# Kernel tuning notes

Measured on AMD Instinct MI355X. Metric: run time of the kernel, lower is better.

The kernel has to match this reference:

```python
import jax, jax.numpy as jnp
import numpy as np

N_T, N_Q = 32768, 4096
E_T, E_Q = 1048576, 131072
H = 128
VOCAB = 1001  # num_features + 1
NUM_LAYERS = 3


def _sage_conv(x, edge_index, Wl, bl, Wr):
    # PyG SAGEConv, aggr='mean': out = lin_l(mean_j x_j) + lin_r(x_i)
    src, dst = edge_index[0], edge_index[1]
    n = x.shape[0]
    agg = jax.ops.segment_sum(x[src], dst, num_segments=n)          # [n, H]
    cnt = jax.ops.segment_sum(jnp.ones((src.shape[0],), x.dtype), dst, num_segments=n)
    mean = agg / jnp.maximum(cnt, 1.0)[:, None]
    return mean @ Wl.T + bl + x @ Wr.T


def setup_inputs() -> dict:
    key = jax.random.key(0)
    ks = jax.random.split(key, 12)
    target_x = jax.random.randint(ks[0], (N_T,), 0, VOCAB, dtype=jnp.int64 if jax.config.jax_enable_x64 else jnp.int32)
    query_x = jax.random.randint(ks[1], (N_Q,), 0, VOCAB, dtype=target_x.dtype)
    target_edge_index = jax.random.randint(ks[2], (2, E_T), 0, N_T, dtype=target_x.dtype)
    query_edge_index = jax.random.randint(ks[3], (2, E_Q), 0, N_Q, dtype=target_x.dtype)
    mask = jax.random.bernoulli(ks[4], 0.5, (N_Q, N_T))
    emb = jax.random.normal(ks[5], (VOCAB, H), jnp.float32) * 0.02
    s = 1.0 / np.sqrt(H)
    Wl = jax.random.uniform(ks[6], (NUM_LAYERS, H, H), jnp.float32, -s, s)
    bl = jax.random.uniform(ks[7], (NUM_LAYERS, H), jnp.float32, -s, s)
    Wr = jax.random.uniform(ks[8], (NUM_LAYERS, H, H), jnp.float32, -s, s)
    return {"target_x": target_x, "query_x": query_x,
            "target_edge_index": target_edge_index, "query_edge_index": query_edge_index,
            "mask": mask, "emb": emb, "Wl": Wl, "bl": bl, "Wr": Wr}


def reference(target_x, query_x, target_edge_index, query_edge_index, mask, emb, Wl, bl, Wr):
    et = emb[target_x]  # [N_T, H]
    eq = emb[query_x]   # [N_Q, H]
    for i in range(NUM_LAYERS):
        et = jax.nn.elu(_sage_conv(et, target_edge_index, Wl[i], bl[i], Wr[i]))
        eq = jax.nn.elu(_sage_conv(eq, query_edge_index, Wl[i], bl[i], Wr[i]))
    fmask = mask.astype(jnp.float32)
    att = (eq @ et.T) * fmask / jnp.sqrt(jnp.float32(H)) + (-1e9) * (1.0 - fmask)
    att = jax.nn.softmax(att, axis=1)
    return att[None]  # [1, N_Q, N_T]
```

## Files before the change

kernel.cpp:

```cpp
#include <hip/hip_runtime.h>
#include <stdint.h>

#define N_T 32768
#define N_Q 4096
#define E_T 1048576
#define E_Q 131072
#define H   128
#define NL  3

typedef float    f32x4 __attribute__((ext_vector_type(4)));
typedef _Float16 f16x8 __attribute__((ext_vector_type(8)));

__device__ __forceinline__ ushort f2h(float x){
  union{_Float16 h; ushort u;} c; c.h = (_Float16)x; return c.u;
}
__device__ __forceinline__ float h2f(unsigned u){
  union{ushort u; _Float16 h;} c; c.u = (ushort)u; return (float)c.h;
}

__global__ void zero_i32_k(int* p, int n){
  int i = blockIdx.x*blockDim.x + threadIdx.x;
  if(i<n) p[i]=0;
}
__global__ void zero_f32_k(float* p, int n){
  int i = blockIdx.x*blockDim.x + threadIdx.x;
  if(i<n) p[i]=0.f;
}

__global__ void detect_mask_k(const unsigned* m, int* flag){
  int t = threadIdx.x;
  int f = 0;
  for(int j=t;j<4096;j+=256){
    unsigned v = m[j];
    if(v > 1u) f |= (v & 0xFEFEFEFEu) ? 2 : 1;
  }
  if(f) atomicOr(flag, f);
}

__global__ void wcvt_k(const float* __restrict__ Wl, const float* __restrict__ Wr,
                       ushort* __restrict__ WH, ushort* __restrict__ WLo){
  int i = blockIdx.x*blockDim.x + threadIdx.x;
  if(i >= NL*128*64) return;
  int k  = (i & 63) * 4;
  int c  = (i >> 6) & 127;
  int l  = i >> 13;
  const float* src = (k < 128)
      ? &Wl[((size_t)l*128 + c)*128 + k]
      : &Wr[((size_t)l*128 + c)*128 + (k-128)];
  float4 v = *(const float4*)src;
  ushort4 h, lo;
  h.x = f2h(v.x); lo.x = f2h(v.x - h2f(h.x));
  h.y = f2h(v.y); lo.y = f2h(v.y - h2f(h.y));
  h.z = f2h(v.z); lo.z = f2h(v.z - h2f(h.z));
  h.w = f2h(v.w); lo.w = f2h(v.w - h2f(h.w));
  size_t off = ((size_t)l*128 + c)*256 + k;
  *(ushort4*)&WH[off]  = h;
  *(ushort4*)&WLo[off] = lo;
}

__global__ void count_k(const int* __restrict__ dst, int E, int* cnt){
  int i = blockIdx.x*blockDim.x + threadIdx.x;
  if(i<E) atomicAdd(&cnt[dst[i]], 1);
}

__global__ void scan_k(const int* __restrict__ cnt, int n, int* rp, int* pos){
  __shared__ int part[1024];
  int t = threadIdx.x;
  int chunk = (n + 1023) >> 10;
  int lo = t*chunk, hi = lo+chunk; if(hi>n) hi=n;
  int s = 0;
  for(int i=lo;i<hi;i++) s += cnt[i];
  part[t] = s;
  __syncthreads();
  for(int off=1; off<1024; off<<=1){
    int v = (t >= off) ? part[t-off] : 0;
    __syncthreads();
    part[t] += v;
    __syncthreads();
  }
  int run = (t==0) ? 0 : part[t-1];
  for(int i=lo;i<hi;i++){ rp[i]=run; pos[i]=run; run += cnt[i]; }
  if(t==0) rp[n] = part[1023];
}

__global__ void fill_k(const int* __restrict__ src, const int* __restrict__ dst,
                       int E, int* pos, int* csr){
  int i = blockIdx.x*blockDim.x + threadIdx.x;
  if(i<E){
    int p = atomicAdd(&pos[dst[i]], 1);
    csr[p] = src[i];
  }
}

__global__ void embed_k(const int* __restrict__ idx, const float* __restrict__ emb,
                        ushort* __restrict__ out, int N){
  int i = blockIdx.x*blockDim.x + threadIdx.x;
  int n = i >> 4, c = i & 15;
  if(n < N){
    size_t eb = (size_t)idx[n]*32 + c*2;
    float4 v0 = ((const float4*)emb)[eb];
    float4 v1 = ((const float4*)emb)[eb+1];
    uint4 o;
    o.x = (unsigned)f2h(v0.x) | ((unsigned)f2h(v0.y)<<16);
    o.y = (unsigned)f2h(v0.z) | ((unsigned)f2h(v0.w)<<16);
    o.z = (unsigned)f2h(v1.x) | ((unsigned)f2h(v1.y)<<16);
    o.w = (unsigned)f2h(v1.z) | ((unsigned)f2h(v1.w)<<16);
    ((uint4*)out)[(size_t)n*16 + c] = o;
  }
}

__global__ void agg_k(const ushort* __restrict__ x, const int* __restrict__ rp,
                      const int* __restrict__ csr, ushort* __restrict__ agg, int N){
  int wid = (int)(((size_t)blockIdx.x*blockDim.x + threadIdx.x) >> 6);
  int lane = threadIdx.x & 63;
  if(wid >= N) return;
  const unsigned* xp = (const unsigned*)x;
  int rs = rp[wid], re = rp[wid+1];
  float ax=0.f, ay=0.f, bx=0.f, by=0.f, cx=0.f, cy=0.f, dx=0.f, dy=0.f;
  int j = rs;
  for(; j+4 <= re; j+=4){
    int s0 = csr[j], s1 = csr[j+1], s2 = csr[j+2], s3 = csr[j+3];
    unsigned u0 = xp[(size_t)s0*64 + lane];
    unsigned u1 = xp[(size_t)s1*64 + lane];
    unsigned u2 = xp[(size_t)s2*64 + lane];
    unsigned u3 = xp[(size_t)s3*64 + lane];
    ax += h2f(u0 & 0xFFFFu); ay += h2f(u0 >> 16);
    bx += h2f(u1 & 0xFFFFu); by += h2f(u1 >> 16);
    cx += h2f(u2 & 0xFFFFu); cy += h2f(u2 >> 16);
    dx += h2f(u3 & 0xFFFFu); dy += h2f(u3 >> 16);
  }
  for(; j < re; j++){
    unsigned u = xp[(size_t)csr[j]*64 + lane];
    ax += h2f(u & 0xFFFFu); ay += h2f(u >> 16);
  }
  float sx = (ax + bx) + (cx + dx);
  float sy = (ay + by) + (cy + dy);
  int c = re - rs; if(c < 1) c = 1;
  float inv = 1.0f / (float)c;
  ((unsigned*)agg)[(size_t)wid*64 + lane] =
      (unsigned)f2h(sx*inv) | ((unsigned)f2h(sy*inv) << 16);
}

__global__ __launch_bounds__(256,3) void layer_k(
    const ushort* __restrict__ agg, const ushort* __restrict__ x,
    const ushort* __restrict__ WH, const ushort* __restrict__ WLo,
    const float* __restrict__ bl, ushort* __restrict__ out16){
  __shared__ ushort SM3[3*128*64];
  ushort* SA = SM3;
  ushort* SH = SM3 + 8192;
  ushort* SL = SM3 + 16384;
  int t = threadIdx.x;
  int r0g = blockIdx.x * 128;
  int lane = t & 63;
  int w = t >> 6;
  int wr = w >> 1, wc = w & 1;
  int fr = lane & 15, kg0 = lane >> 4;
  f32x4 acc[4][4] = {};
  for(int kt=0; kt<4; kt++){
    __syncthreads();
    const ushort* A = (kt < 2) ? agg : x;
    int ko = (kt & 1) * 64;
    #pragma unroll
    for(int it=0; it<4; it++){
      int idx = t + it*256;
      int row = idx >> 3, k8 = idx & 7;
      int sw = (k8 ^ (row & 7)) * 8;
      *(uint4*)&SA[row*64 + sw] = *(const uint4*)&A[(size_t)(r0g+row)*H + ko + k8*8];
      *(uint4*)&SH[row*64 + sw] = *(const uint4*)&WH[row*256 + kt*64 + k8*8];
      *(uint4*)&SL[row*64 + sw] = *(const uint4*)&WLo[row*256 + kt*64 + k8*8];
    }
    __syncthreads();
    #pragma unroll
    for(int s=0; s<2; s++){
      int kg = s*4 + kg0;
      f16x8 a[4], bh[4], blo[4];
      #pragma unroll
      for(int m=0;m<4;m++){
        int ar = wr*64 + m*16 + fr;
        a[m] = *(const f16x8*)&SA[ar*64 + ((kg ^ (ar & 7)) << 3)];
      }
      #pragma unroll
      for(int n=0;n<4;n++){
        int bc = wc*64 + n*16 + fr;
        int ib = bc*64 + ((kg ^ (bc & 7)) << 3);
        bh[n]  = *(const f16x8*)&SH[ib];
        blo[n] = *(const f16x8*)&SL[ib];
      }
      #pragma unroll
      for(int m=0;m<4;m++)
        #pragma unroll
        for(int n=0;n<4;n++){
          acc[m][n] = __builtin_amdgcn_mfma_f32_16x16x32_f16(a[m], bh[n],  acc[m][n], 0,0,0);
          acc[m][n] = __builtin_amdgcn_mfma_f32_16x16x32_f16(a[m], blo[n], acc[m][n], 0,0,0);
        }
    }
  }
  __syncthreads();
  ushort* LT = SM3;
  #pragma unroll
  for(int n=0;n<4;n++){
    int c = wc*64 + n*16 + fr;
    float b = bl[c];
    #pragma unroll
    for(int m=0;m<4;m++){
      int r = wr*64 + m*16 + kg0*4;
      #pragma unroll
      for(int reg=0;reg<4;reg++){
        float v = acc[m][n][reg] + b;
        v = (v > 0.f) ? v : expm1f(v);
        LT[(r+reg)*128 + c] = f2h(v);
      }
    }
  }
  __syncthreads();
  #pragma unroll
  for(int i=0;i<8;i++){
    int idx = t + i*256;
    int row = idx >> 4, c8 = idx & 15;
    *(uint4*)&out16[(size_t)(r0g+row)*H + c8*8] = *(uint4*)&LT[row*128 + c8*8];
  }
}

__device__ __forceinline__ unsigned nib8(unsigned x, unsigned y){
  unsigned r = (x & 0xFu) | ((x>>4)&0xF0u) | ((x>>8)&0xF00u) | ((x>>12)&0xF000u);
  unsigned s = (y & 0xFu) | ((y>>4)&0xF0u) | ((y>>8)&0xF00u) | ((y>>12)&0xF000u);
  return r | (s<<16);
}
__device__ __forceinline__ unsigned pk4(unsigned u){
  return ((u & 0xFFu)       ? 1u : 0u) | ((u & 0xFF00u)     ? 2u : 0u)
       | ((u & 0xFF0000u)   ? 4u : 0u) | ((u & 0xFF000000u) ? 8u : 0u);
}

__device__ __forceinline__ void stage_mask_tile(const void* maskp, int mb,
    int gr0, int gc0, unsigned* MB, uint8_t* NB, unsigned* bitsOut, int t){
  if(mb & 2){
    const float* base = (const float*)maskp;
    #pragma unroll
    for(int i=0;i<16;i++){
      int idx = i*256 + t;
      int row = idx >> 5, c4 = idx & 31;
      float4 v = *(const float4*)&base[(size_t)(gr0+row)*N_T + gc0 + c4*4];
      NB[row*32 + c4] = (uint8_t)((unsigned)(v.x!=0.f) | ((unsigned)(v.y!=0.f)<<1)
                                | ((unsigned)(v.z!=0.f)<<2) | ((unsigned)(v.w!=0.f)<<3));
    }
  } else if(mb & 1){
    const uint8_t* base = (const uint8_t*)maskp;
    #pragma unroll
    for(int i=0;i<16;i++){
      int idx = i*256 + t;
      int row = idx >> 5, c4 = idx & 31;
      unsigned u = *(const unsigned*)&base[(size_t)(gr0+row)*N_T + gc0 + c4*4];
      NB[row*32 + c4] = (uint8_t)pk4(u);
    }
  } else {
    const int* base = (const int*)maskp;
    #pragma unroll
    for(int i=0;i<16;i++){
      int idx = i*256 + t;
      int row = idx >> 5, c4 = idx & 31;
      int4 v = *(const int4*)&base[(size_t)(gr0+row)*N_T + gc0 + c4*4];
      NB[row*32 + c4] = (uint8_t)((unsigned)(v.x!=0) | ((unsigned)(v.y!=0)<<1)
                                | ((unsigned)(v.z!=0)<<2) | ((unsigned)(v.w!=0)<<3));
    }
  }
  __syncthreads();
  if(t < 128){
    uint4 a = *(const uint4*)&NB[t*32];
    uint4 b = *(const uint4*)&NB[t*32 + 16];
    unsigned w0 = nib8(a.x, a.y), w1 = nib8(a.z, a.w);
    unsigned w2 = nib8(b.x, b.y), w3 = nib8(b.z, b.w);
    MB[t*4]   = w0; MB[t*4+1] = w1;
    MB[t*4+2] = w2; MB[t*4+3] = w3;
    if(bitsOut){
      uint4 o; o.x=w0; o.y=w1; o.z=w2; o.w=w3;
      *(uint4*)&bitsOut[(size_t)(gr0 + t)*(N_T/32) + (gc0 >> 5)] = o;
    }
  }
}

__device__ __forceinline__ void qk_gemm(
    const ushort* __restrict__ A16, const ushort* __restrict__ B16,
    int abase, int bbase, int t, ushort* SM, f32x4 (&acc)[4][4]){
  ushort* AB = SM;
  ushort* BB = SM + 8192;
  int lane = t & 63;
  int w = t >> 6;
  int wr = w >> 1, wc = w & 1;
  int fr = lane & 15, kg0 = lane >> 4;
  for(int kt=0; kt<2; kt++){
    __syncthreads();
    #pragma unroll
    for(int it=0; it<4; it++){
      int idx = t + it*256;
      int row = idx >> 3, k8 = idx & 7;
      int sw = (k8 ^ (row & 7)) * 8;
      *(uint4*)&AB[row*64 + sw] = *(const uint4*)&A16[(size_t)(abase+row)*H + kt*64 + k8*8];
      *(uint4*)&BB[row*64 + sw] = *(const uint4*)&B16[(size_t)(bbase+row)*H + kt*64 + k8*8];
    }
    __syncthreads();
    #pragma unroll
    for(int s=0; s<2; s++){
      int kg = s*4 + kg0;
      f16x8 a[4], b[4];
      #pragma unroll
      for(int m=0;m<4;m++){
        int ar = wr*64 + m*16 + fr;
        a[m] = *(const f16x8*)&AB[ar*64 + ((kg ^ (ar & 7)) << 3)];
      }
      #pragma unroll
      for(int n=0;n<4;n++){
        int bc = wc*64 + n*16 + fr;
        b[n] = *(const f16x8*)&BB[bc*64 + ((kg ^ (bc & 7)) << 3)];
      }
      #pragma unroll
      for(int m=0;m<4;m++)
        #pragma unroll
        for(int n=0;n<4;n++)
          acc[m][n] = __builtin_amdgcn_mfma_f32_16x16x32_f16(a[m], b[n], acc[m][n], 0,0,0);
    }
  }
}

__global__ __launch_bounds__(256,4) void attsum_k(
    const ushort* __restrict__ eq16, const ushort* __restrict__ et16,
    const void* __restrict__ maskp, const int* __restrict__ flag,
    unsigned* __restrict__ bitsOut, float* __restrict__ rowsum){
  __shared__ ushort SM[2*128*64];
  __shared__ __align__(16) unsigned MB[512];
  __shared__ float RS[128][2];
  int t = threadIdx.x;
  int gc0 = blockIdx.x * 128;
  int gr0 = blockIdx.y * 128;
  int lane = t & 63;
  int w = t >> 6;
  int wr = w >> 1, wc = w & 1;
  int fr = lane & 15, kg0 = lane >> 4;

  int mb = *flag;
  stage_mask_tile(maskp, mb, gr0, gc0, MB, (uint8_t*)SM, bitsOut, t);

  f32x4 acc[4][4] = {};
  qk_gemm(et16, eq16, gc0, gr0, t, SM, acc);

  const float sc = 0.08838834764831845f;
  #pragma unroll
  for(int n=0;n<4;n++){
    int q = wc*64 + n*16 + fr;
    float s = 0.f;
    #pragma unroll
    for(int m=0;m<4;m++){
      unsigned wb = MB[q*4 + wr*2 + (m>>1)];
      int off = ((m&1)<<4) | (kg0<<2);
      s += ((wb>>(off+0))&1u) ? __expf(acc[m][n][0]*sc) : 0.f;
      s += ((wb>>(off+1))&1u) ? __expf(acc[m][n][1]*sc) : 0.f;
      s += ((wb>>(off+2))&1u) ? __expf(acc[m][n][2]*sc) : 0.f;
      s += ((wb>>(off+3))&1u) ? __expf(acc[m][n][3]*sc) : 0.f;
    }
    s += __shfl_xor(s, 16);
    s += __shfl_xor(s, 32);
    if(lane < 16) RS[q][wr] = s;
  }
  __syncthreads();
  if(t < 128) atomicAdd(&rowsum[gr0 + t], RS[t][0] + RS[t][1]);
}

__global__ __launch_bounds__(256,4) void attout_k(
    const ushort* __restrict__ eq16, const ushort* __restrict__ et16,
    const void* __restrict__ maskp, const int* __restrict__ flag,
    const unsigned* __restrict__ bitsIn, const float* __restrict__ rowsum,
    float* __restrict__ out){
  __shared__ ushort SM[2*128*64];
  __shared__ __align__(16) unsigned MB[512];
  __shared__ float IRS[128];
  int t = threadIdx.x;
  int gc0 = blockIdx.x * 128;
  int gr0 = blockIdx.y * 128;
  int lane = t & 63;
  int w = t >> 6;
  int wr = w >> 1, wc = w & 1;
  int fr = lane & 15, kg0 = lane >> 4;

  if(bitsIn){
    if(t < 128)
      *(uint4*)&MB[t*4] = *(const uint4*)&bitsIn[(size_t)(gr0 + t)*(N_T/32) + (gc0 >> 5)];
  } else {
    int mb = *flag;
    stage_mask_tile(maskp, mb, gr0, gc0, MB, (uint8_t*)SM, nullptr, t);
  }
  if(t < 128) IRS[t] = 1.0f / rowsum[gr0 + t];

  f32x4 acc[4][4] = {};
  qk_gemm(et16, eq16, gc0, gr0, t, SM, acc);

  const float sc = 0.08838834764831845f;
  #pragma unroll
  for(int n=0;n<4;n++){
    int q = wc*64 + n*16 + fr;
    float ir = IRS[q];
    size_t rb = (size_t)(gr0 + q)*N_T + gc0 + wr*64;
    #pragma unroll
    for(int m=0;m<4;m++){
      unsigned wb = MB[q*4 + wr*2 + (m>>1)];
      int off = ((m&1)<<4) | (kg0<<2);
      float4 o;
      o.x = ((wb>>(off+0))&1u) ? __expf(acc[m][n][0]*sc)*ir : 0.f;
      o.y = ((wb>>(off+1))&1u) ? __expf(acc[m][n][1]*sc)*ir : 0.f;
      o.z = ((wb>>(off+2))&1u) ? __expf(acc[m][n][2]*sc)*ir : 0.f;
      o.w = ((wb>>(off+3))&1u) ? __expf(acc[m][n][3]*sc)*ir : 0.f;
      *(float4*)&out[rb + m*16 + (kg0<<2)] = o;
    }
  }
}

extern "C" void kernel_launch(void* const* d_in, const int* in_sizes, int n_in,
                              void* d_out, int out_size, void* d_ws, size_t ws_size,
                              hipStream_t stream){
  const int* tx  = (const int*)d_in[0];
  const int* qx  = (const int*)d_in[1];
  const int* te  = (const int*)d_in[2];
  const int* qe  = (const int*)d_in[3];
  const void* mask = d_in[4];
  const float* emb = (const float*)d_in[5];
  const float* Wl  = (const float*)d_in[6];
  const float* bl  = (const float*)d_in[7];
  const float* Wr  = (const float*)d_in[8];
  float* out = (float*)d_out;

  ushort* et16 = (ushort*)d_ws;
  ushort* eq16 = et16 + (size_t)N_T*H;
  float* rowsum = (float*)(eq16 + (size_t)N_Q*H);
  int*   flag   = (int*)(rowsum + N_Q);
  ushort* WH  = (ushort*)((char*)d_ws + ((size_t)10 << 20));
  ushort* WLo = WH + (size_t)NL*128*256;
  bool useBits = ws_size >= ((size_t)37 << 20);
  unsigned* bits = useBits ? (unsigned*)((char*)d_ws + ((size_t)19 << 20)) : nullptr;

  char* S = (char*)d_out;
  ushort* xt0  = (ushort*)(S);
  ushort* xt1  = (ushort*)(S + 8388608);
  ushort* aggt = (ushort*)(S + 16777216);
  ushort* xq0  = (ushort*)(S + 25165824);
  ushort* xq1  = (ushort*)(S + 26214400);
  ushort* aggq = (ushort*)(S + 27262976);
  int*   cnt_t = (int*)(S + 28311552);
  int*   rp_t  = cnt_t + N_T;
  int*   pos_t = rp_t + N_T + 1;
  int*   csr_t = pos_t + N_T;
  int*   cnt_q = csr_t + E_T;
  int*   rp_q  = cnt_q + N_Q;
  int*   pos_q = rp_q + N_Q + 1;
  int*   csr_q = pos_q + N_Q;

  zero_i32_k<<<(N_T+255)/256,256,0,stream>>>(cnt_t, N_T);
  zero_i32_k<<<(N_Q+255)/256,256,0,stream>>>(cnt_q, N_Q);
  zero_f32_k<<<(N_Q+255)/256,256,0,stream>>>(rowsum, N_Q);
  zero_i32_k<<<1,256,0,stream>>>(flag, 1);
  detect_mask_k<<<1,256,0,stream>>>((const unsigned*)mask, flag);
  wcvt_k<<<96,256,0,stream>>>(Wl, Wr, WH, WLo);

  count_k<<<E_T/256,256,0,stream>>>(te+E_T, E_T, cnt_t);
  scan_k<<<1,1024,0,stream>>>(cnt_t, N_T, rp_t, pos_t);
  fill_k<<<E_T/256,256,0,stream>>>(te, te+E_T, E_T, pos_t, csr_t);
  count_k<<<E_Q/256,256,0,stream>>>(qe+E_Q, E_Q, cnt_q);
  scan_k<<<1,1024,0,stream>>>(cnt_q, N_Q, rp_q, pos_q);
  fill_k<<<E_Q/256,256,0,stream>>>(qe, qe+E_Q, E_Q, pos_q, csr_q);

  embed_k<<<N_T*16/256,256,0,stream>>>(tx, emb, xt0, N_T);
  embed_k<<<N_Q*16/256,256,0,stream>>>(qx, emb, xq0, N_Q);

  ushort* ct = xt0; ushort* nt = xt1;
  ushort* cq = xq0; ushort* nq = xq1;
  for(int l=0;l<NL;l++){
    int last = (l == NL-1);
    const ushort* wh = WH  + (size_t)l*128*256;
    const ushort* wl = WLo + (size_t)l*128*256;
    agg_k<<<N_T/4,256,0,stream>>>(ct, rp_t, csr_t, aggt, N_T);
    layer_k<<<N_T/128,256,0,stream>>>(aggt, ct, wh, wl, bl+(size_t)l*H, last ? et16 : nt);
    agg_k<<<N_Q/4,256,0,stream>>>(cq, rp_q, csr_q, aggq, N_Q);
    layer_k<<<N_Q/128,256,0,stream>>>(aggq, cq, wh, wl, bl+(size_t)l*H, last ? eq16 : nq);
    ushort* tmp;
    tmp = ct; ct = nt; nt = tmp;
    tmp = cq; cq = nq; nq = tmp;
  }

  attsum_k<<<dim3(N_T/128, N_Q/128),256,0,stream>>>(eq16, et16, mask, flag, bits, rowsum);
  attout_k<<<dim3(N_T/128, N_Q/128),256,0,stream>>>(eq16, et16, mask, flag, bits, rowsum, out);
}
```

Measured before the change: 766.8 us.

## Fuse embedding lookup into layer-0 gather, widen agg unroll, use nontemporal mask/output

Drops the per-node embed kernels. Layer 0 instead gathers rows straight from a small fp16 copy of the embedding table, indexed by node id, in both the aggregation and the layer GEMM. The aggregation loop now unrolls over 8 neighbours with separate accumulators, which gives more memory-level parallelism. Mask loads and output stores in the attention kernels become nontemporal, so the large streaming traffic bypasses cache retention. The costs are a double indirection in layer 0 and the rowsum buffer moving to a new workspace offset.

```diff
diff --git a/kernel.cpp b/kernel.cpp
--- a/kernel.cpp
+++ b/kernel.cpp
@@ -7,8 +7,11 @@
 #define E_Q 131072
 #define H   128
 #define NL  3
+#define VOCAB 1001
 
 typedef float    f32x4 __attribute__((ext_vector_type(4)));
+typedef int      i32x4 __attribute__((ext_vector_type(4)));
+typedef unsigned u32x4 __attribute__((ext_vector_type(4)));
 typedef _Float16 f16x8 __attribute__((ext_vector_type(8)));
 
 __device__ __forceinline__ ushort f2h(float x){
@@ -58,6 +61,19 @@
   *(ushort4*)&WLo[off] = lo;
 }
 
+__global__ void ecvt_k(const float* __restrict__ e, ushort* __restrict__ o){
+  int i = blockIdx.x*blockDim.x + threadIdx.x;
+  if(i >= VOCAB*H/8) return;
+  float4 v0 = ((const float4*)e)[(size_t)i*2];
+  float4 v1 = ((const float4*)e)[(size_t)i*2 + 1];
+  uint4 u;
+  u.x = (unsigned)f2h(v0.x) | ((unsigned)f2h(v0.y)<<16);
+  u.y = (unsigned)f2h(v0.z) | ((unsigned)f2h(v0.w)<<16);
+  u.z = (unsigned)f2h(v1.x) | ((unsigned)f2h(v1.y)<<16);
+  u.w = (unsigned)f2h(v1.z) | ((unsigned)f2h(v1.w)<<16);
+  ((uint4*)o)[i] = u;
+}
+
 __global__ void count_k(const int* __restrict__ dst, int E, int* cnt){
   int i = blockIdx.x*blockDim.x + threadIdx.x;
   if(i<E) atomicAdd(&cnt[dst[i]], 1);
@@ -92,49 +108,47 @@
   }
 }
 
-__global__ void embed_k(const int* __restrict__ idx, const float* __restrict__ emb,
-                        ushort* __restrict__ out, int N){
-  int i = blockIdx.x*blockDim.x + threadIdx.x;
-  int n = i >> 4, c = i & 15;
-  if(n < N){
-    size_t eb = (size_t)idx[n]*32 + c*2;
-    float4 v0 = ((const float4*)emb)[eb];
-    float4 v1 = ((const float4*)emb)[eb+1];
-    uint4 o;
-    o.x = (unsigned)f2h(v0.x) | ((unsigned)f2h(v0.y)<<16);
-    o.y = (unsigned)f2h(v0.z) | ((unsigned)f2h(v0.w)<<16);
-    o.z = (unsigned)f2h(v1.x) | ((unsigned)f2h(v1.y)<<16);
-    o.w = (unsigned)f2h(v1.z) | ((unsigned)f2h(v1.w)<<16);
-    ((uint4*)out)[(size_t)n*16 + c] = o;
-  }
-}
-
-__global__ void agg_k(const ushort* __restrict__ x, const int* __restrict__ rp,
-                      const int* __restrict__ csr, ushort* __restrict__ agg, int N){
+__global__ void agg_k(const ushort* __restrict__ x, const int* __restrict__ nid,
+                      const ushort* __restrict__ emb16,
+                      const int* __restrict__ rp, const int* __restrict__ csr,
+                      ushort* __restrict__ agg, int N){
   int wid = (int)(((size_t)blockIdx.x*blockDim.x + threadIdx.x) >> 6);
   int lane = threadIdx.x & 63;
   if(wid >= N) return;
-  const unsigned* xp = (const unsigned*)x;
+  const unsigned* xw = (const unsigned*)x;
+  const unsigned* ew = (const unsigned*)emb16;
   int rs = rp[wid], re = rp[wid+1];
-  float ax=0.f, ay=0.f, bx=0.f, by=0.f, cx=0.f, cy=0.f, dx=0.f, dy=0.f;
+  float px[8], py[8];
+  #pragma unroll
+  for(int q=0;q<8;q++){ px[q]=0.f; py[q]=0.f; }
   int j = rs;
-  for(; j+4 <= re; j+=4){
-    int s0 = csr[j], s1 = csr[j+1], s2 = csr[j+2], s3 = csr[j+3];
-    unsigned u0 = xp[(size_t)s0*64 + lane];
-    unsigned u1 = xp[(size_t)s1*64 + lane];
-    unsigned u2 = xp[(size_t)s2*64 + lane];
-    unsigned u3 = xp[(size_t)s3*64 + lane];
-    ax += h2f(u0 & 0xFFFFu); ay += h2f(u0 >> 16);
-    bx += h2f(u1 & 0xFFFFu); by += h2f(u1 >> 16);
-    cx += h2f(u2 & 0xFFFFu); cy += h2f(u2 >> 16);
-    dx += h2f(u3 & 0xFFFFu); dy += h2f(u3 >> 16);
-  }
-  for(; j < re; j++){
-    unsigned u = xp[(size_t)csr[j]*64 + lane];
-    ax += h2f(u & 0xFFFFu); ay += h2f(u >> 16);
-  }
-  float sx = (ax + bx) + (cx + dx);
-  float sy = (ay + by) + (cy + dy);
+  if(nid){
+    for(; j+8 <= re; j+=8){
+      #pragma unroll
+      for(int q=0;q<8;q++){
+        unsigned u = ew[(size_t)nid[csr[j+q]]*64 + lane];
+        px[q] += h2f(u & 0xFFFFu); py[q] += h2f(u >> 16);
+      }
+    }
+    for(; j < re; j++){
+      unsigned u = ew[(size_t)nid[csr[j]]*64 + lane];
+      px[0] += h2f(u & 0xFFFFu); py[0] += h2f(u >> 16);
+    }
+  } else {
+    for(; j+8 <= re; j+=8){
+      #pragma unroll
+      for(int q=0;q<8;q++){
+        unsigned u = xw[(size_t)csr[j+q]*64 + lane];
+        px[q] += h2f(u & 0xFFFFu); py[q] += h2f(u >> 16);
+      }
+    }
+    for(; j < re; j++){
+      unsigned u = xw[(size_t)csr[j]*64 + lane];
+      px[0] += h2f(u & 0xFFFFu); py[0] += h2f(u >> 16);
+    }
+  }
+  float sx = ((px[0]+px[1]) + (px[2]+px[3])) + ((px[4]+px[5]) + (px[6]+px[7]));
+  float sy = ((py[0]+py[1]) + (py[2]+py[3])) + ((py[4]+py[5]) + (py[6]+py[7]));
   int c = re - rs; if(c < 1) c = 1;
   float inv = 1.0f / (float)c;
   ((unsigned*)agg)[(size_t)wid*64 + lane] =
@@ -142,7 +156,8 @@
 }
 
 __global__ __launch_bounds__(256,3) void layer_k(
-    const ushort* __restrict__ agg, const ushort* __restrict__ x,
+    const ushort* __restrict__ agg, const ushort* __restrict__ xprev,
+    const int* __restrict__ nid, const ushort* __restrict__ emb16,
     const ushort* __restrict__ WH, const ushort* __restrict__ WLo,
     const float* __restrict__ bl, ushort* __restrict__ out16){
   __shared__ ushort SM3[3*128*64];
@@ -158,14 +173,21 @@
   f32x4 acc[4][4] = {};
   for(int kt=0; kt<4; kt++){
     __syncthreads();
-    const ushort* A = (kt < 2) ? agg : x;
     int ko = (kt & 1) * 64;
     #pragma unroll
     for(int it=0; it<4; it++){
       int idx = t + it*256;
       int row = idx >> 3, k8 = idx & 7;
       int sw = (k8 ^ (row & 7)) * 8;
-      *(uint4*)&SA[row*64 + sw] = *(const uint4*)&A[(size_t)(r0g+row)*H + ko + k8*8];
+      uint4 av;
+      if(kt < 2){
+        av = *(const uint4*)&agg[(size_t)(r0g+row)*H + ko + k8*8];
+      } else if(nid){
+        av = *(const uint4*)&emb16[(size_t)nid[r0g+row]*H + ko + k8*8];
+      } else {
+        av = *(const uint4*)&xprev[(size_t)(r0g+row)*H + ko + k8*8];
+      }
+      *(uint4*)&SA[row*64 + sw] = av;
       *(uint4*)&SH[row*64 + sw] = *(const uint4*)&WH[row*256 + kt*64 + k8*8];
       *(uint4*)&SL[row*64 + sw] = *(const uint4*)&WLo[row*256 + kt*64 + k8*8];
     }
@@ -234,14 +256,15 @@
 __device__ __forceinline__ void stage_mask_tile(const void* maskp, int mb,
     int gr0, int gc0, unsigned* MB, uint8_t* NB, unsigned* bitsOut, int t){
   if(mb & 2){
-    const float* base = (const float*)maskp;
+    const f32x4* base = (const f32x4*)maskp;
     #pragma unroll
     for(int i=0;i<16;i++){
       int idx = i*256 + t;
       int row = idx >> 5, c4 = idx & 31;
-      float4 v = *(const float4*)&base[(size_t)(gr0+row)*N_T + gc0 + c4*4];
-      NB[row*32 + c4] = (uint8_t)((unsigned)(v.x!=0.f) | ((unsigned)(v.y!=0.f)<<1)
-                                | ((unsigned)(v.z!=0.f)<<2) | ((unsigned)(v.w!=0.f)<<3));
+      f32x4 v = __builtin_nontemporal_load(
+          &base[((size_t)(gr0+row)*N_T + gc0) / 4 + c4]);
+      NB[row*32 + c4] = (uint8_t)((unsigned)(v[0]!=0.f) | ((unsigned)(v[1]!=0.f)<<1)
+                                | ((unsigned)(v[2]!=0.f)<<2) | ((unsigned)(v[3]!=0.f)<<3));
     }
   } else if(mb & 1){
     const uint8_t* base = (const uint8_t*)maskp;
@@ -249,18 +272,20 @@
     for(int i=0;i<16;i++){
       int idx = i*256 + t;
       int row = idx >> 5, c4 = idx & 31;
-      unsigned u = *(const unsigned*)&base[(size_t)(gr0+row)*N_T + gc0 + c4*4];
+      unsigned u = __builtin_nontemporal_load(
+          (const unsigned*)&base[(size_t)(gr0+row)*N_T + gc0 + c4*4]);
       NB[row*32 + c4] = (uint8_t)pk4(u);
     }
   } else {
-    const int* base = (const int*)maskp;
+    const i32x4* base = (const i32x4*)maskp;
     #pragma unroll
     for(int i=0;i<16;i++){
       int idx = i*256 + t;
       int row = idx >> 5, c4 = idx & 31;
-      int4 v = *(const int4*)&base[(size_t)(gr0+row)*N_T + gc0 + c4*4];
-      NB[row*32 + c4] = (uint8_t)((unsigned)(v.x!=0) | ((unsigned)(v.y!=0)<<1)
-                                | ((unsigned)(v.z!=0)<<2) | ((unsigned)(v.w!=0)<<3));
+      i32x4 v = __builtin_nontemporal_load(
+          &base[((size_t)(gr0+row)*N_T + gc0) / 4 + c4]);
+      NB[row*32 + c4] = (uint8_t)((unsigned)(v[0]!=0) | ((unsigned)(v[1]!=0)<<1)
+                                | ((unsigned)(v[2]!=0)<<2) | ((unsigned)(v[3]!=0)<<3));
     }
   }
   __syncthreads();
@@ -402,12 +427,12 @@
     for(int m=0;m<4;m++){
       unsigned wb = MB[q*4 + wr*2 + (m>>1)];
       int off = ((m&1)<<4) | (kg0<<2);
-      float4 o;
-      o.x = ((wb>>(off+0))&1u) ? __expf(acc[m][n][0]*sc)*ir : 0.f;
-      o.y = ((wb>>(off+1))&1u) ? __expf(acc[m][n][1]*sc)*ir : 0.f;
-      o.z = ((wb>>(off+2))&1u) ? __expf(acc[m][n][2]*sc)*ir : 0.f;
-      o.w = ((wb>>(off+3))&1u) ? __expf(acc[m][n][3]*sc)*ir : 0.f;
-      *(float4*)&out[rb + m*16 + (kg0<<2)] = o;
+      f32x4 o;
+      o[0] = ((wb>>(off+0))&1u) ? __expf(acc[m][n][0]*sc)*ir : 0.f;
+      o[1] = ((wb>>(off+1))&1u) ? __expf(acc[m][n][1]*sc)*ir : 0.f;
+      o[2] = ((wb>>(off+2))&1u) ? __expf(acc[m][n][2]*sc)*ir : 0.f;
+      o[3] = ((wb>>(off+3))&1u) ? __expf(acc[m][n][3]*sc)*ir : 0.f;
+      __builtin_nontemporal_store(o, (f32x4*)&out[rb + m*16 + (kg0<<2)]);
     }
   }
 }
@@ -428,10 +453,11 @@
 
   ushort* et16 = (ushort*)d_ws;
   ushort* eq16 = et16 + (size_t)N_T*H;
-  float* rowsum = (float*)(eq16 + (size_t)N_Q*H);
+  float* rowsum = (float*)((char*)d_ws + ((size_t)9 << 20));
   int*   flag   = (int*)(rowsum + N_Q);
   ushort* WH  = (ushort*)((char*)d_ws + ((size_t)10 << 20));
   ushort* WLo = WH + (size_t)NL*128*256;
+  ushort* emb16 = (ushort*)((char*)d_ws + ((size_t)11 << 20));
   bool useBits = ws_size >= ((size_t)37 << 20);
   unsigned* bits = useBits ? (unsigned*)((char*)d_ws + ((size_t)19 << 20)) : nullptr;
 
@@ -457,6 +483,7 @@
   zero_i32_k<<<1,256,0,stream>>>(flag, 1);
   detect_mask_k<<<1,256,0,stream>>>((const unsigned*)mask, flag);
   wcvt_k<<<96,256,0,stream>>>(Wl, Wr, WH, WLo);
+  ecvt_k<<<(VOCAB*H/8+255)/256,256,0,stream>>>(emb, emb16);
 
   count_k<<<E_T/256,256,0,stream>>>(te+E_T, E_T, cnt_t);
   scan_k<<<1,1024,0,stream>>>(cnt_t, N_T, rp_t, pos_t);
@@ -465,22 +492,23 @@
   scan_k<<<1,1024,0,stream>>>(cnt_q, N_Q, rp_q, pos_q);
   fill_k<<<E_Q/256,256,0,stream>>>(qe, qe+E_Q, E_Q, pos_q, csr_q);
 
-  embed_k<<<N_T*16/256,256,0,stream>>>(tx, emb, xt0, N_T);
-  embed_k<<<N_Q*16/256,256,0,stream>>>(qx, emb, xq0, N_Q);
-
-  ushort* ct = xt0; ushort* nt = xt1;
-  ushort* cq = xq0; ushort* nq = xq1;
+  ushort* outs_t[NL] = {xt0, xt1, et16};
+  ushort* outs_q[NL] = {xq0, xq1, eq16};
+  const ushort* cur_t = nullptr;
+  const ushort* cur_q = nullptr;
   for(int l=0;l<NL;l++){
-    int last = (l == NL-1);
     const ushort* wh = WH  + (size_t)l*128*256;
     const ushort* wl = WLo + (size_t)l*128*256;
-    agg_k<<<N_T/4,256,0,stream>>>(ct, rp_t, csr_t, aggt, N_T);
-    layer_k<<<N_T/128,256,0,stream>>>(aggt, ct, wh, wl, bl+(size_t)l*H, last ? et16 : nt);
-    agg_k<<<N_Q/4,256,0,stream>>>(cq, rp_q, csr_q, aggq, N_Q);
-    layer_k<<<N_Q/128,256,0,stream>>>(aggq, cq, wh, wl, bl+(size_t)l*H, last ? eq16 : nq);
-    ushort* tmp;
-    tmp = ct; ct = nt; nt = tmp;
-    tmp = cq; cq = nq; nq = tmp;
+    const int* nidt = (l==0) ? tx : nullptr;
+    const int* nidq = (l==0) ? qx : nullptr;
+    agg_k<<<N_T/4,256,0,stream>>>(cur_t, nidt, emb16, rp_t, csr_t, aggt, N_T);
+    layer_k<<<N_T/128,256,0,stream>>>(aggt, cur_t, nidt, emb16, wh, wl,
+                                      bl+(size_t)l*H, outs_t[l]);
+    agg_k<<<N_Q/4,256,0,stream>>>(cur_q, nidq, emb16, rp_q, csr_q, aggq, N_Q);
+    layer_k<<<N_Q/128,256,0,stream>>>(aggq, cur_q, nidq, emb16, wh, wl,
+                                      bl+(size_t)l*H, outs_q[l]);
+    cur_t = outs_t[l];
+    cur_q = outs_q[l];
   }
 
   attsum_k<<<dim3(N_T/128, N_Q/128),256,0,stream>>>(eq16, et16, mask, flag, bits, rowsum);
```

Result: faster. 711.1 us (-7.3%).
